# Kernel tuning notes

Measured on AMD Instinct MI355X. Metric: run time of the kernel, lower is better.

## Reference

```python
import jax, jax.numpy as jnp
import numpy as np

B, C, N_ELEM = 16, 256, 8192
N_FILT, N_DIL = 2, 256


def setup_inputs() -> dict:
    key = jax.random.key(0)
    kx, kw = jax.random.split(key)
    x = jax.random.normal(kx, (B, C, N_ELEM), dtype=jnp.float32)
    # xavier_uniform on a (n_out, n_in, n_filt) tensor: fan_in = fan_out = C * N_FILT
    fan = C * N_FILT
    bound = float(np.sqrt(6.0 / (fan + fan)))
    weight = jax.random.uniform(kw, (C, C, N_FILT), minval=-bound, maxval=bound, dtype=jnp.float32)
    return {"x": x, "weight": weight, "n_dil": N_DIL}


def reference(x, weight, n_dil):
    # x: (B, C_in, N); weight: (C_out, C_in, n_filt); requires C_out == C_in.
    n_out, n_in, n_filt = weight.shape
    filter_size = (n_filt - 1) * n_dil + 1
    n_steps = x.shape[2] - filter_size

    # The torch loop computes, for i in [0, n_steps):
    #   x[:, :, i+1] = sum_{c,k} weight[o, c, k] * x_read[:, c, i + k*n_dil]
    # where the k=0 tap reads the UPDATED x (written at step i-1) and all
    # k>=1 taps read the ORIGINAL x (those positions are written at later
    # steps, and torch evaluates the conv before the in-place write).
    # => affine recurrence: s[i+1] = W0 @ s[i] + c[i], s[0] = x[:, :, 0].

    # c[t] = sum_{k>=1} W_k @ x_orig[:, :, t + k*n_dil]  -> (n_steps, B, C_out)
    c = jnp.zeros((n_steps, x.shape[0], n_out), dtype=x.dtype)
    for k in range(1, n_filt):
        xk = x[:, :, k * n_dil: k * n_dil + n_steps]  # (B, C_in, n_steps)
        c = c + jnp.einsum('oc,bct->tbo', weight[:, :, k], xk)

    W0T = weight[:, :, 0].T  # (C_in, C_out)

    def step(state, ct):
        # state: (B, C); ct: (B, C)
        new = state @ W0T + ct
        return new, new

    _, ys = jax.lax.scan(step, x[:, :, 0], c)  # ys: (n_steps, B, C)
    x_out = x.at[:, :, 1:1 + n_steps].set(jnp.transpose(ys, (1, 2, 0)))
    return x_out
```

## Files before the change

### kernel.cpp

```cpp
#include <hip/hip_runtime.h>
#include <stdint.h>


constexpr int BATCH  = 16;
constexpr int CH     = 256;
constexpr int NEL    = 8192;
constexpr int NDIL   = 256;
constexpr int TSTEPS = NEL - (NDIL + 1);
constexpr int LCH    = 16;
constexpr int NCH    = (TSTEPS + LCH - 1) / LCH;
constexpr int OUT_L  = 32;
constexpr int WARM   = 20;
constexpr int NCH2   = (TSTEPS + OUT_L - 1) / OUT_L;
constexpr int TPB    = 256;
constexpr int YPAD   = 260;
constexpr int A2PAD  = 264;
constexpr int TTILES = (TSTEPS + 127) / 128;
constexpr int YROW   = 264;

constexpr size_t OFF_AF    = 0;
constexpr size_t OFF_P1    = OFF_AF    + 256 * 1024;
constexpr size_t OFF_P2    = OFF_P1    + 256 * 1024;
constexpr size_t OFF_AB16  = OFF_P2    + 256 * 1024;
constexpr size_t OFF_W1B   = OFF_AB16  + 128 * 1024;
constexpr size_t OFF_E     = OFF_W1B   + 128 * 1024;
constexpr size_t OFF_INIT  = OFF_E     + (size_t)NCH * BATCH * CH * 4;
constexpr size_t OFF_AFRAG = OFF_INIT  + (size_t)(NCH + 1) * BATCH * CH * 4;
constexpr size_t OFF_W1FR  = OFF_AFRAG + 128 * 1024;
constexpr size_t OFF_CBUF  = OFF_W1FR  + 128 * 1024;
constexpr size_t CBUF_BYTES = (size_t)(NCH * LCH) * BATCH * CH * 2;
constexpr size_t OFF_YBUF  = OFF_CBUF + CBUF_BYTES;
constexpr size_t WS_NEED   = OFF_YBUF + CBUF_BYTES;

typedef __attribute__((ext_vector_type(8))) short bf16x8;
typedef __attribute__((ext_vector_type(4))) float f32x4;

__device__ __forceinline__ float bfu(uint32_t hibits) { return __uint_as_float(hibits); }
__device__ __forceinline__ float bf2f(uint16_t b) { return __uint_as_float(((uint32_t)b) << 16); }
__device__ __forceinline__ uint16_t f2bf(float f) {
  uint32_t u = __float_as_uint(f);
  uint32_t r = u + 0x7fffu + ((u >> 16) & 1u);
  return (uint16_t)(r >> 16);
}

__global__ void k_prep(const float* __restrict__ w, float* __restrict__ Af,
                       uint16_t* __restrict__ Ab, uint16_t* __restrict__ W1b,
                       uint16_t* __restrict__ Afrag, uint16_t* __restrict__ W1f) {
  int o = blockIdx.x, c = threadIdx.x;
  const float2 wv = *(const float2*)&w[(size_t)(o * CH + c) * 2];
  Af[c * CH + o]  = wv.x;
  Ab[c * CH + o]  = f2bf(wv.x);
  W1b[c * CH + o] = f2bf(wv.y);
  if (Afrag) {
    int kb = c >> 5, g = (c >> 3) & 3, ii = c & 7;
    int nt = o >> 4, mm = o & 15;
    size_t idx = (((size_t)(kb * 16 + nt) * 64) + (g * 16 + mm)) * 8 + ii;
    Afrag[idx] = f2bf(wv.x);
    W1f[idx]   = f2bf(wv.y);
  }
}

__global__ void k_init0(const float* __restrict__ x, float* __restrict__ initbuf) {
  int b = blockIdx.x, c = threadIdx.x;
  initbuf[b * CH + c] = x[(size_t)(b * CH + c) * NEL];
}

__global__ __launch_bounds__(TPB) void k_sqmm(const float* __restrict__ in,
                                              float* __restrict__ outm) {
  __shared__ __align__(16) float row[CH];
  int r = blockIdx.x, o = threadIdx.x;
  row[o] = in[r * CH + o];
  __syncthreads();
  float acc = 0.f;
#pragma unroll 8
  for (int k = 0; k < CH; ++k) acc += row[k] * in[k * CH + o];
  outm[r * CH + o] = acc;
}

__global__ void k_edges(const float* __restrict__ x, float* __restrict__ out) {
  size_t base = (size_t)blockIdx.x * NEL;
  int t = threadIdx.x;
  out[base + (NEL - 256) + t] = x[base + (NEL - 256) + t];
  if (t == 0) out[base] = x[base];
}

__global__ __launch_bounds__(512, 4) void k_cgemm_m(const float* __restrict__ x,
                                                    const uint16_t* __restrict__ W1f,
                                                    uint16_t* __restrict__ cb,
                                                    float* __restrict__ out) {
  __shared__ __align__(16) uint16_t Axs[64 * 64 * 8];
  int tid = threadIdx.x, bid = blockIdx.x;
  if (bid >= BATCH * TTILES) {
    int b = bid - BATCH * TTILES;
    int o = tid >> 1, half = tid & 1;
    size_t rbase = (size_t)(b * CH + o) * NEL;
    const float* src = &x[rbase + (NEL - 256) + half * 128];
    float* dst = &out[rbase + (NEL - 256) + half * 128];
#pragma unroll
    for (int i = 0; i < 32; ++i)
      *(float4*)&dst[i * 4] = *(const float4*)&src[i * 4];
    if (half == 0) out[rbase] = x[rbase];
    return;
  }
  int b = bid / TTILES, tt = bid % TTILES;
  int t0 = tt * 128;
  int w = tid >> 6, l = tid & 63, lm = l & 15, g = l >> 4;
  const float* xb = x + (size_t)b * CH * NEL + (t0 + NDIL);

  bf16x8 bv[8][2];
#pragma unroll
  for (int kb = 0; kb < 8; ++kb)
#pragma unroll
    for (int p = 0; p < 2; ++p)
      bv[kb][p] =
          *(const bf16x8*)&W1f[(((size_t)(kb * 16 + w * 2 + p) * 64) + l) * 8];

  int tA = w * 16 + lm;
#pragma unroll
  for (int kq = 0; kq < 4; ++kq) {
    float v[2][8];
#pragma unroll
    for (int k2 = 0; k2 < 2; ++k2)
#pragma unroll
      for (int i = 0; i < 8; ++i)
        v[k2][i] = xb[(size_t)((kq * 2 + k2) * 32 + g * 8 + i) * NEL + tA];
#pragma unroll
    for (int k2 = 0; k2 < 2; ++k2) {
      uint4 pk;
      pk.x = (uint32_t)f2bf(v[k2][0]) | ((uint32_t)f2bf(v[k2][1]) << 16);
      pk.y = (uint32_t)f2bf(v[k2][2]) | ((uint32_t)f2bf(v[k2][3]) << 16);
      pk.z = (uint32_t)f2bf(v[k2][4]) | ((uint32_t)f2bf(v[k2][5]) << 16);
      pk.w = (uint32_t)f2bf(v[k2][6]) | ((uint32_t)f2bf(v[k2][7]) << 16);
      *(uint4*)&Axs[((w * 8 + kq * 2 + k2) * 64 + l) * 8] = pk;
    }
  }
  __syncthreads();

#pragma unroll 1
  for (int mt = 0; mt < 8; ++mt) {
    f32x4 acc0 = (f32x4)0.f, acc1 = (f32x4)0.f;
#pragma unroll
    for (int kb = 0; kb < 8; ++kb) {
      bf16x8 av = *(const bf16x8*)&Axs[((mt * 8 + kb) * 64 + l) * 8];
      acc0 = __builtin_amdgcn_mfma_f32_16x16x32_bf16(av, bv[kb][0], acc0, 0, 0, 0);
      acc1 = __builtin_amdgcn_mfma_f32_16x16x32_bf16(av, bv[kb][1], acc1, 0, 0, 0);
    }
#pragma unroll
    for (int r = 0; r < 4; ++r) {
      int t2 = t0 + mt * 16 + g * 4 + r;
      if (t2 < TSTEPS) {
        size_t base = (size_t)t2 * (BATCH * CH) + b * CH;
        cb[base + (w * 2 + 0) * 16 + lm] = f2bf(acc0[r]);
        cb[base + (w * 2 + 1) * 16 + lm] = f2bf(acc1[r]);
      }
    }
  }
}

__device__ __forceinline__ void scan2_step(
    int t, bool pref, bool doout, const uint16_t* Yr, uint16_t* Yw,
    const uint16_t* __restrict__ cb, uint16_t* __restrict__ yb,
    const bf16x8 af[8][4], ushort* cc, int w, int lm, int g, int tid) {
  bf16x8 yv[8];
#pragma unroll
  for (int kb = 0; kb < 8; ++kb)
    yv[kb] = *(const bf16x8*)&Yr[lm * YROW + kb * 32 + g * 8];
  f32x4 acc[4];
#pragma unroll
  for (int ntl = 0; ntl < 4; ++ntl)
#pragma unroll
    for (int r = 0; r < 4; ++r)
      acc[ntl][r] = bfu(((uint32_t)cc[ntl * 4 + r]) << 16);
  if (pref) {
    size_t cbase = (size_t)(t + 2) * (BATCH * CH);
#pragma unroll
    for (int ntl = 0; ntl < 4; ++ntl)
#pragma unroll
      for (int r = 0; r < 4; ++r)
        cc[ntl * 4 + r] = cb[cbase + (g * 4 + r) * CH + (w * 4 + ntl) * 16 + lm];
  }
#pragma unroll
  for (int ntl = 0; ntl < 4; ++ntl) {
#pragma unroll
    for (int kb = 0; kb < 8; ++kb)
      acc[ntl] = __builtin_amdgcn_mfma_f32_16x16x32_bf16(yv[kb], af[kb][ntl], acc[ntl], 0, 0, 0);
  }
  uint16_t hbv[16];
#pragma unroll
  for (int ntl = 0; ntl < 4; ++ntl)
#pragma unroll
    for (int r = 0; r < 4; ++r) {
      float v = acc[ntl][r];
      int bb = g * 4 + r, o = (w * 4 + ntl) * 16 + lm;
      uint16_t hb = f2bf(v);
      hbv[ntl * 4 + r] = hb;
      Yw[bb * YROW + o] = hb;
    }
  if (doout) {
    uint4 p0, p1;
    p0.x = (uint32_t)hbv[0] | ((uint32_t)hbv[1] << 16);
    p0.y = (uint32_t)hbv[2] | ((uint32_t)hbv[3] << 16);
    p0.z = (uint32_t)hbv[4] | ((uint32_t)hbv[5] << 16);
    p0.w = (uint32_t)hbv[6] | ((uint32_t)hbv[7] << 16);
    p1.x = (uint32_t)hbv[8] | ((uint32_t)hbv[9] << 16);
    p1.y = (uint32_t)hbv[10] | ((uint32_t)hbv[11] << 16);
    p1.z = (uint32_t)hbv[12] | ((uint32_t)hbv[13] << 16);
    p1.w = (uint32_t)hbv[14] | ((uint32_t)hbv[15] << 16);
    uint4* dst = (uint4*)&yb[(size_t)t * 4096 + tid * 16];
    dst[0] = p0;
    dst[1] = p1;
  }
  asm volatile("s_waitcnt lgkmcnt(0)" ::: "memory");
  __builtin_amdgcn_sched_barrier(0);
  __builtin_amdgcn_s_barrier();
  __builtin_amdgcn_sched_barrier(0);
}

__global__ __launch_bounds__(TPB, 2) void k_scan2(
    const uint16_t* __restrict__ Afrag, const uint16_t* __restrict__ cb,
    uint16_t* __restrict__ yb, const float* __restrict__ x) {
  __shared__ __align__(16) uint16_t Y[2][16 * YROW];
  int tid = threadIdx.x;
  int j = blockIdx.x;
  int w = tid >> 6, l = tid & 63;
  int lm = l & 15, g = l >> 4;

  bf16x8 af[8][4];
#pragma unroll
  for (int kb = 0; kb < 8; ++kb)
#pragma unroll
    for (int ntl = 0; ntl < 4; ++ntl) {
      int nt = w * 4 + ntl;
      af[kb][ntl] = *(const bf16x8*)&Afrag[(((size_t)(kb * 16 + nt) * 64) + l) * 8];
    }

  int tstart   = (j == 0) ? 0 : OUT_L * j - WARM;
  int outstart = OUT_L * j;
  int tend     = min(OUT_L * (j + 1), TSTEPS);

  if (j == 0) {
    int b = tid >> 4, o0 = (tid & 15) * 16;
#pragma unroll
    for (int q = 0; q < 16; ++q)
      Y[0][b * YROW + o0 + q] = f2bf(x[(size_t)(b * CH + o0 + q) * NEL]);
  } else {
    for (int q = tid; q < 16 * YROW; q += TPB) Y[0][q] = 0;
  }

  ushort c0[16], c1[16];
  {
#pragma unroll
    for (int ntl = 0; ntl < 4; ++ntl)
#pragma unroll
      for (int r = 0; r < 4; ++r) {
        size_t off = (size_t)(g * 4 + r) * CH + (w * 4 + ntl) * 16 + lm;
        c0[ntl * 4 + r] = cb[(size_t)tstart * (BATCH * CH) + off];
        c1[ntl * 4 + r] = cb[(size_t)(tstart + 1) * (BATCH * CH) + off];
      }
  }
  __syncthreads();

#pragma unroll 1
  for (int ii = 0; ii < OUT_L + WARM + 2; ii += 2) {
    int t = tstart + ii;
    if (t >= tend) break;
    scan2_step(t, t + 2 < tend, t >= outstart, Y[0], Y[1], cb, yb,
               af, c0, w, lm, g, tid);
    if (t + 1 >= tend) break;
    scan2_step(t + 1, t + 3 < tend, t + 1 >= outstart, Y[1], Y[0], cb, yb,
               af, c1, w, lm, g, tid);
  }
}

__global__ __launch_bounds__(TPB) void k_yout(const uint16_t* __restrict__ yb,
                                              float* __restrict__ out) {
  __shared__ __align__(16) uint16_t t2[256 * 72];
  int bid = blockIdx.x;
  int tb = bid >> 4, sub = bid & 15;
  int G = sub >> 2, wS = sub & 3;
  int t0 = tb * 64;
  int tid = threadIdx.x;
  {
    int tl = tid >> 2, part = tid & 3;
    int ty = t0 + tl - 1;
    if (ty >= 0) {
      const uint16_t* src =
          &yb[(size_t)ty * 4096 + (wS * 64 + G * 16) * 16 + part * 64];
#pragma unroll
      for (int i = 0; i < 8; ++i) {
        uint4 vv = *(const uint4*)&src[i * 8];
        uint32_t uu[4] = {vv.x, vv.y, vv.z, vv.w};
        int colb = part * 64 + i * 8;
#pragma unroll
        for (int e = 0; e < 4; ++e) {
          t2[(colb + 2 * e) * 72 + tl]     = (uint16_t)(uu[e] & 0xffffu);
          t2[(colb + 2 * e + 1) * 72 + tl] = (uint16_t)(uu[e] >> 16);
        }
      }
    }
  }
  __syncthreads();
  {
    int b = G * 4 + (tid >> 6);
    int o = wS * 64 + (tid & 63);
    int col = (o & 15) * 16 + ((o >> 4) & 3) * 4 + (b & 3);
    float* dst = &out[(size_t)(b * CH + o) * NEL + t0];
#pragma unroll
    for (int k4 = 0; k4 < 4; ++k4) {
      uint4 v0 = *(const uint4*)&t2[col * 72 + k4 * 16];
      uint4 v1 = *(const uint4*)&t2[col * 72 + k4 * 16 + 8];
      uint32_t uu[8] = {v0.x, v0.y, v0.z, v0.w, v1.x, v1.y, v1.z, v1.w};
      float f[16];
#pragma unroll
      for (int e = 0; e < 8; ++e) {
        f[2 * e]     = bfu(uu[e] << 16);
        f[2 * e + 1] = bfu(uu[e] & 0xffff0000u);
      }
      if (tb == 0 && k4 == 0) {
#pragma unroll
        for (int e = 1; e < 16; ++e) dst[e] = f[e];
      } else {
#pragma unroll
        for (int m = 0; m < 4; ++m)
          *(float4*)&dst[k4 * 16 + m * 4] =
              make_float4(f[4 * m], f[4 * m + 1], f[4 * m + 2], f[4 * m + 3]);
      }
    }
  }
}

__global__ __launch_bounds__(TPB) void k_cgemm_v(const float* __restrict__ x,
                                                 const uint16_t* __restrict__ W1b,
                                                 float* __restrict__ out) {
  __shared__ __align__(16) uint16_t w1[CH * 128];
  __shared__ __align__(16) float xs[32][128];
  int tid = threadIdx.x;
  int bid = blockIdx.x;
  int b = bid / (TTILES * 2);
  int rem = bid % (TTILES * 2);
  int ttile = rem >> 1, otile = rem & 1;
  int t0 = ttile * 128, o0 = otile * 128;
  int tx = tid & 15, ty = tid >> 4;
  int o8 = o0 + tx * 8;
  int tb = t0 + ty * 8;
  {
    uint4* dst = (uint4*)w1;
    for (int q = tid; q < CH * 128 / 8; q += TPB) {
      int row = q >> 4, seg = q & 15;
      dst[q] = *(const uint4*)&W1b[row * CH + o0 + seg * 8];
    }
  }
  float acc[8][8];
#pragma unroll
  for (int i = 0; i < 8; ++i)
#pragma unroll
    for (int j = 0; j < 8; ++j) acc[i][j] = 0.f;
  for (int c0 = 0; c0 < CH; c0 += 32) {
    __syncthreads();
#pragma unroll
    for (int kk = 0; kk < 4; ++kk) {
      int q = tid + kk * TPB;
      int cc = q >> 5, tf = (q & 31) * 4;
      *(float4*)&xs[cc][tf] =
          *(const float4*)&x[(size_t)(b * CH + c0 + cc) * NEL + t0 + NDIL + tf];
    }
    __syncthreads();
#pragma unroll 4
    for (int cc = 0; cc < 32; ++cc) {
      float4 xa = *(const float4*)&xs[cc][ty * 8];
      float4 xb = *(const float4*)&xs[cc][ty * 8 + 4];
      float xv[8] = {xa.x, xa.y, xa.z, xa.w, xb.x, xb.y, xb.z, xb.w};
      uint4 wv = *(const uint4*)&w1[(c0 + cc) * 128 + tx * 8];
      float wf[8] = {bfu(wv.x << 16), bfu(wv.x & 0xffff0000u),
                     bfu(wv.y << 16), bfu(wv.y & 0xffff0000u),
                     bfu(wv.z << 16), bfu(wv.z & 0xffff0000u),
                     bfu(wv.w << 16), bfu(wv.w & 0xffff0000u)};
#pragma unroll
      for (int i = 0; i < 8; ++i)
#pragma unroll
        for (int j = 0; j < 8; ++j) acc[i][j] += xv[i] * wf[j];
    }
  }
#pragma unroll
  for (int j = 0; j < 8; ++j) {
    size_t base = (size_t)(b * CH + o8 + j) * NEL + tb + 1;
#pragma unroll
    for (int i = 0; i < 8; ++i)
      if (tb + i < TSTEPS) out[base + i] = acc[i][j];
  }
}

template <bool PH3>
__global__ __launch_bounds__(TPB) void k_scan(const uint16_t* __restrict__ Ab,
                                              const float* __restrict__ initbuf,
                                              float* __restrict__ Ebuf,
                                              float* __restrict__ out) {
  __shared__ __align__(16) uint16_t Al[CH * CH];
  __shared__ __align__(16) float yl[BATCH * YPAD];
  int tid = threadIdx.x;
  int j = blockIdx.x;
  {
    const uint4* src = (const uint4*)Ab;
    uint4* dst = (uint4*)Al;
    for (int q = tid; q < CH * CH / 8; q += TPB) dst[q] = src[q];
  }
  if constexpr (PH3) {
    for (int q = tid; q < BATCH * CH / 4; q += TPB) {
      int b = q >> 6, c4 = (q & 63) * 4;
      *(float4*)&yl[b * YPAD + c4] =
          *(const float4*)&initbuf[(size_t)j * BATCH * CH + b * CH + c4];
    }
  } else {
    for (int q = tid; q < BATCH * YPAD; q += TPB) yl[q] = 0.f;
  }
  __syncthreads();
  int o4 = (tid & 63) * 4;
  int b4 = (tid >> 6) * 4;
  int len = min(LCH, TSTEPS - j * LCH);
  float acc[4][4];
  for (int i = 0; i < len; ++i) {
    int t = j * LCH + i;
    float cv[4][4];
#pragma unroll
    for (int bb = 0; bb < 4; ++bb)
#pragma unroll
      for (int oo = 0; oo < 4; ++oo)
        cv[bb][oo] = out[(size_t)((b4 + bb) * CH + o4 + oo) * NEL + t + 1];
#pragma unroll
    for (int bb = 0; bb < 4; ++bb)
#pragma unroll
      for (int oo = 0; oo < 4; ++oo) acc[bb][oo] = 0.f;
#pragma unroll 2
    for (int c = 0; c < CH; c += 4) {
      float4 v0 = *(const float4*)&yl[(b4 + 0) * YPAD + c];
      float4 v1 = *(const float4*)&yl[(b4 + 1) * YPAD + c];
      float4 v2 = *(const float4*)&yl[(b4 + 2) * YPAD + c];
      float4 v3 = *(const float4*)&yl[(b4 + 3) * YPAD + c];
      float y0[4] = {v0.x, v0.y, v0.z, v0.w};
      float y1[4] = {v1.x, v1.y, v1.z, v1.w};
      float y2[4] = {v2.x, v2.y, v2.z, v2.w};
      float y3[4] = {v3.x, v3.y, v3.z, v3.w};
#pragma unroll
      for (int k = 0; k < 4; ++k) {
        uint2 au = *(const uint2*)&Al[(c + k) * CH + o4];
        float a[4] = {bfu(au.x << 16), bfu(au.x & 0xffff0000u),
                      bfu(au.y << 16), bfu(au.y & 0xffff0000u)};
#pragma unroll
        for (int oo = 0; oo < 4; ++oo) {
          acc[0][oo] += y0[k] * a[oo];
          acc[1][oo] += y1[k] * a[oo];
          acc[2][oo] += y2[k] * a[oo];
          acc[3][oo] += y3[k] * a[oo];
        }
      }
    }
#pragma unroll
    for (int bb = 0; bb < 4; ++bb)
#pragma unroll
      for (int oo = 0; oo < 4; ++oo) acc[bb][oo] += cv[bb][oo];
    __syncthreads();
#pragma unroll
    for (int bb = 0; bb < 4; ++bb)
      *(float4*)&yl[(b4 + bb) * YPAD + o4] =
          make_float4(acc[bb][0], acc[bb][1], acc[bb][2], acc[bb][3]);
    if constexpr (PH3) {
#pragma unroll
      for (int bb = 0; bb < 4; ++bb)
#pragma unroll
        for (int oo = 0; oo < 4; ++oo)
          out[(size_t)((b4 + bb) * CH + o4 + oo) * NEL + t + 1] = acc[bb][oo];
    }
    __syncthreads();
  }
  if constexpr (!PH3) {
#pragma unroll
    for (int bb = 0; bb < 4; ++bb)
#pragma unroll
      for (int oo = 0; oo < 4; ++oo)
        Ebuf[(size_t)j * BATCH * CH + (b4 + bb) * CH + o4 + oo] = acc[bb][oo];
  }
}

__global__ __launch_bounds__(TPB) void k_phase2(const float* __restrict__ ALf,
                                                const float* __restrict__ Ebuf,
                                                float* __restrict__ initbuf) {
  __shared__ __align__(16) uint16_t At[CH * A2PAD];
  __shared__ __align__(16) float st[CH];
  int b = blockIdx.x, tid = threadIdx.x;
  for (int q = tid; q < CH * CH; q += TPB) {
    int c = q >> 8, o = q & 255;
    At[o * A2PAD + c] = f2bf(ALf[q]);
  }
  st[tid] = initbuf[b * CH + tid];
  __syncthreads();
  for (int jj = 1; jj < NCH; ++jj) {
    float acc = Ebuf[(size_t)(jj - 1) * BATCH * CH + b * CH + tid];
#pragma unroll 4
    for (int c = 0; c < CH; c += 8) {
      uint4 au = *(const uint4*)&At[tid * A2PAD + c];
      float4 s0 = *(const float4*)&st[c];
      float4 s1 = *(const float4*)&st[c + 4];
      acc += bfu(au.x << 16) * s0.x + bfu(au.x & 0xffff0000u) * s0.y +
             bfu(au.y << 16) * s0.z + bfu(au.y & 0xffff0000u) * s0.w +
             bfu(au.z << 16) * s1.x + bfu(au.z & 0xffff0000u) * s1.y +
             bfu(au.w << 16) * s1.z + bfu(au.w & 0xffff0000u) * s1.w;
    }
    __syncthreads();
    st[tid] = acc;
    initbuf[(size_t)jj * BATCH * CH + b * CH + tid] = acc;
    __syncthreads();
  }
}

extern "C" void kernel_launch(void* const* d_in, const int* in_sizes, int n_in,
                              void* d_out, int out_size, void* d_ws, size_t ws_size,
                              hipStream_t stream) {
  const float* x = (const float*)d_in[0];
  const float* w = (const float*)d_in[1];
  float* out = (float*)d_out;
  char* ws = (char*)d_ws;

  float*    Af    = (float*)(ws + OFF_AF);
  float*    P1    = (float*)(ws + OFF_P1);
  float*    P2    = (float*)(ws + OFF_P2);
  uint16_t* Ab    = (uint16_t*)(ws + OFF_AB16);
  uint16_t* W1b   = (uint16_t*)(ws + OFF_W1B);
  float*    Ebuf  = (float*)(ws + OFF_E);
  float*    inb   = (float*)(ws + OFF_INIT);
  uint16_t* Afrag = (uint16_t*)(ws + OFF_AFRAG);
  uint16_t* W1f   = (uint16_t*)(ws + OFF_W1FR);
  uint16_t* cbuf  = (uint16_t*)(ws + OFF_CBUF);
  uint16_t* ybuf  = (uint16_t*)(ws + OFF_YBUF);

  const bool fast = ws_size >= WS_NEED;

  k_prep<<<CH, CH, 0, stream>>>(w, Af, Ab, W1b, fast ? Afrag : nullptr, W1f);
  if (fast) {
    k_cgemm_m<<<BATCH * TTILES + BATCH, 512, 0, stream>>>(x, W1f, cbuf, out);
    k_scan2<<<NCH2, TPB, 0, stream>>>(Afrag, cbuf, ybuf, x);
    k_yout<<<124 * 16, TPB, 0, stream>>>(ybuf, out);
  } else {
    k_edges<<<BATCH * CH, 256, 0, stream>>>(x, out);
    k_init0<<<BATCH, CH, 0, stream>>>(x, inb);
    k_sqmm<<<CH, TPB, 0, stream>>>(Af, P1);
    k_sqmm<<<CH, TPB, 0, stream>>>(P1, P2);
    k_sqmm<<<CH, TPB, 0, stream>>>(P2, P1);
    k_sqmm<<<CH, TPB, 0, stream>>>(P1, P2);
    k_cgemm_v<<<BATCH * TTILES * 2, TPB, 0, stream>>>(x, W1b, out);
    k_scan<false><<<NCH - 1, TPB, 0, stream>>>(Ab, nullptr, Ebuf, out);
    k_phase2<<<BATCH, TPB, 0, stream>>>(P2, Ebuf, inb);
    k_scan<true><<<NCH, TPB, 0, stream>>>(Ab, inb, nullptr, out);
  }
}
```

Measured before the change: 191.9 us.

## Fuse output transpose into scan kernel via LDS ring buffer; halve cgemm time tile

The scan kernel now stages each step's bf16 results in a 16-slot shared-memory ring and, every 16 steps, transposes and writes them straight to the fp32 output. This removes the separate k_yout kernel and the global y buffer round trip. The C-GEMM kernel also moves to 64-step time tiles, launching twice as many blocks with smaller shared memory. The trade-off is 128KB of extra LDS in the scan kernel, which drops it to one block per CU, plus extra barriers during flushes.

Result: slower. 205.1 us (+6.9%).

```diff
diff --git a/kernel.cpp b/kernel.cpp
--- a/kernel.cpp
+++ b/kernel.cpp
@@ -16,6 +16,7 @@
 constexpr int YPAD   = 260;
 constexpr int A2PAD  = 264;
 constexpr int TTILES = (TSTEPS + 127) / 128;
+constexpr int TT64   = 124;
 constexpr int YROW   = 264;
 
 constexpr size_t OFF_AF    = 0;
@@ -29,8 +30,7 @@
 constexpr size_t OFF_W1FR  = OFF_AFRAG + 128 * 1024;
 constexpr size_t OFF_CBUF  = OFF_W1FR  + 128 * 1024;
 constexpr size_t CBUF_BYTES = (size_t)(NCH * LCH) * BATCH * CH * 2;
-constexpr size_t OFF_YBUF  = OFF_CBUF + CBUF_BYTES;
-constexpr size_t WS_NEED   = OFF_YBUF + CBUF_BYTES;
+constexpr size_t WS_NEED   = OFF_CBUF + CBUF_BYTES;
 
 typedef __attribute__((ext_vector_type(8))) short bf16x8;
 typedef __attribute__((ext_vector_type(4))) float f32x4;
@@ -88,10 +88,10 @@
                                                     const uint16_t* __restrict__ W1f,
                                                     uint16_t* __restrict__ cb,
                                                     float* __restrict__ out) {
-  __shared__ __align__(16) uint16_t Axs[64 * 64 * 8];
+  __shared__ __align__(16) uint16_t Axs[32 * 64 * 8];
   int tid = threadIdx.x, bid = blockIdx.x;
-  if (bid >= BATCH * TTILES) {
-    int b = bid - BATCH * TTILES;
+  if (bid >= BATCH * TT64) {
+    int b = bid - BATCH * TT64;
     int o = tid >> 1, half = tid & 1;
     size_t rbase = (size_t)(b * CH + o) * NEL;
     const float* src = &x[rbase + (NEL - 256) + half * 128];
@@ -102,8 +102,8 @@
     if (half == 0) out[rbase] = x[rbase];
     return;
   }
-  int b = bid / TTILES, tt = bid % TTILES;
-  int t0 = tt * 128;
+  int b = bid / TT64, tt = bid % TT64;
+  int t0 = tt * 64;
   int w = tid >> 6, l = tid & 63, lm = l & 15, g = l >> 4;
   const float* xb = x + (size_t)b * CH * NEL + (t0 + NDIL);
 
@@ -115,29 +115,29 @@
       bv[kb][p] =
           *(const bf16x8*)&W1f[(((size_t)(kb * 16 + w * 2 + p) * 64) + l) * 8];
 
-  int tA = w * 16 + lm;
-#pragma unroll
-  for (int kq = 0; kq < 4; ++kq) {
-    float v[2][8];
-#pragma unroll
-    for (int k2 = 0; k2 < 2; ++k2)
+  {
+    int mt_s = w & 3, kb0 = (w >> 2) * 4;
+    int tA = mt_s * 16 + lm;
+    float v[4][8];
+#pragma unroll
+    for (int k2 = 0; k2 < 4; ++k2)
 #pragma unroll
       for (int i = 0; i < 8; ++i)
-        v[k2][i] = xb[(size_t)((kq * 2 + k2) * 32 + g * 8 + i) * NEL + tA];
-#pragma unroll
-    for (int k2 = 0; k2 < 2; ++k2) {
+        v[k2][i] = xb[(size_t)((kb0 + k2) * 32 + g * 8 + i) * NEL + tA];
+#pragma unroll
+    for (int k2 = 0; k2 < 4; ++k2) {
       uint4 pk;
       pk.x = (uint32_t)f2bf(v[k2][0]) | ((uint32_t)f2bf(v[k2][1]) << 16);
       pk.y = (uint32_t)f2bf(v[k2][2]) | ((uint32_t)f2bf(v[k2][3]) << 16);
       pk.z = (uint32_t)f2bf(v[k2][4]) | ((uint32_t)f2bf(v[k2][5]) << 16);
       pk.w = (uint32_t)f2bf(v[k2][6]) | ((uint32_t)f2bf(v[k2][7]) << 16);
-      *(uint4*)&Axs[((w * 8 + kq * 2 + k2) * 64 + l) * 8] = pk;
+      *(uint4*)&Axs[((mt_s * 8 + kb0 + k2) * 64 + l) * 8] = pk;
     }
   }
   __syncthreads();
 
 #pragma unroll 1
-  for (int mt = 0; mt < 8; ++mt) {
+  for (int mt = 0; mt < 4; ++mt) {
     f32x4 acc0 = (f32x4)0.f, acc1 = (f32x4)0.f;
 #pragma unroll
     for (int kb = 0; kb < 8; ++kb) {
@@ -157,9 +157,9 @@
   }
 }
 
-__device__ __forceinline__ void scan2_step(
-    int t, bool pref, bool doout, const uint16_t* Yr, uint16_t* Yw,
-    const uint16_t* __restrict__ cb, uint16_t* __restrict__ yb,
+__device__ __forceinline__ void scan3_step(
+    int t, bool pref, const uint16_t* Yr, uint16_t* Yw,
+    const uint16_t* __restrict__ cb, uint16_t (*R)[4096],
     const bf16x8 af[8][4], ushort* cc, int w, int lm, int g, int tid) {
   bf16x8 yv[8];
 #pragma unroll
@@ -196,7 +196,7 @@
       hbv[ntl * 4 + r] = hb;
       Yw[bb * YROW + o] = hb;
     }
-  if (doout) {
+  {
     uint4 p0, p1;
     p0.x = (uint32_t)hbv[0] | ((uint32_t)hbv[1] << 16);
     p0.y = (uint32_t)hbv[2] | ((uint32_t)hbv[3] << 16);
@@ -206,9 +206,9 @@
     p1.y = (uint32_t)hbv[10] | ((uint32_t)hbv[11] << 16);
     p1.z = (uint32_t)hbv[12] | ((uint32_t)hbv[13] << 16);
     p1.w = (uint32_t)hbv[14] | ((uint32_t)hbv[15] << 16);
-    uint4* dst = (uint4*)&yb[(size_t)t * 4096 + tid * 16];
-    dst[0] = p0;
-    dst[1] = p1;
+    uint16_t* slice = R[t & 15];
+    *(uint4*)&slice[tid * 8] = p0;
+    *(uint4*)&slice[2048 + tid * 8] = p1;
   }
   asm volatile("s_waitcnt lgkmcnt(0)" ::: "memory");
   __builtin_amdgcn_sched_barrier(0);
@@ -216,10 +216,51 @@
   __builtin_amdgcn_sched_barrier(0);
 }
 
-__global__ __launch_bounds__(TPB, 2) void k_scan2(
+__device__ __forceinline__ void scan3_flush(int t, const uint16_t (*R)[4096],
+                                            float* __restrict__ out, int tid) {
+  int ob = t - 14;
+  int o = tid;
+#pragma unroll
+  for (int ii = 0; ii < 16; ii += 2) {
+    int ttw = (o >> 6) * 64 + (ii >> 2) * 16 + (o & 15);
+    int f   = ((o >> 4) & 3) * 4 + (ii & 3);
+    int pos = ((f & 8) ? 2048 : 0) + ttw * 8 + (f & 7);
+    float fa[16], fb[16];
+#pragma unroll
+    for (int q = 0; q < 16; ++q) {
+      uint32_t u = *(const uint32_t*)&R[(q + 15) & 15][pos];
+      fa[q] = bfu(u << 16);
+      fb[q] = bfu(u & 0xffff0000u);
+    }
+    float* dA = &out[(size_t)(ii * CH + o) * NEL + ob];
+    float* dB = &out[(size_t)((ii + 1) * CH + o) * NEL + ob];
+    if (ob == 0) {
+      dA[1] = fa[1]; dA[2] = fa[2]; dA[3] = fa[3];
+      dB[1] = fb[1]; dB[2] = fb[2]; dB[3] = fb[3];
+#pragma unroll
+      for (int m = 1; m < 4; ++m) {
+        *(float4*)&dA[m * 4] = make_float4(fa[4*m], fa[4*m+1], fa[4*m+2], fa[4*m+3]);
+        *(float4*)&dB[m * 4] = make_float4(fb[4*m], fb[4*m+1], fb[4*m+2], fb[4*m+3]);
+      }
+    } else {
+#pragma unroll
+      for (int m = 0; m < 4; ++m) {
+        *(float4*)&dA[m * 4] = make_float4(fa[4*m], fa[4*m+1], fa[4*m+2], fa[4*m+3]);
+        *(float4*)&dB[m * 4] = make_float4(fb[4*m], fb[4*m+1], fb[4*m+2], fb[4*m+3]);
+      }
+    }
+  }
+  asm volatile("s_waitcnt lgkmcnt(0)" ::: "memory");
+  __builtin_amdgcn_sched_barrier(0);
+  __builtin_amdgcn_s_barrier();
+  __builtin_amdgcn_sched_barrier(0);
+}
+
+__global__ __launch_bounds__(TPB, 1) void k_scan3(
     const uint16_t* __restrict__ Afrag, const uint16_t* __restrict__ cb,
-    uint16_t* __restrict__ yb, const float* __restrict__ x) {
+    float* __restrict__ out, const float* __restrict__ x) {
   __shared__ __align__(16) uint16_t Y[2][16 * YROW];
+  __shared__ __align__(16) uint16_t R[16][4096];
   int tid = threadIdx.x;
   int j = blockIdx.x;
   int w = tid >> 6, l = tid & 63;
@@ -236,7 +277,7 @@
 
   int tstart   = (j == 0) ? 0 : OUT_L * j - WARM;
   int outstart = OUT_L * j;
-  int tend     = min(OUT_L * (j + 1), TSTEPS);
+  int tend     = min(OUT_L * j + OUT_L - 1, TSTEPS);
 
   if (j == 0) {
     int b = tid >> 4, o0 = (tid & 15) * 16;
@@ -261,71 +302,14 @@
   __syncthreads();
 
 #pragma unroll 1
-  for (int ii = 0; ii < OUT_L + WARM + 2; ii += 2) {
-    int t = tstart + ii;
+  for (int ii2 = 0; ii2 < OUT_L + WARM + 2; ii2 += 2) {
+    int t = tstart + ii2;
     if (t >= tend) break;
-    scan2_step(t, t + 2 < tend, t >= outstart, Y[0], Y[1], cb, yb,
-               af, c0, w, lm, g, tid);
+    scan3_step(t, t + 2 < tend, Y[0], Y[1], cb, R, af, c0, w, lm, g, tid);
+    if (t >= outstart && (t & 15) == 14) scan3_flush(t, R, out, tid);
     if (t + 1 >= tend) break;
-    scan2_step(t + 1, t + 3 < tend, t + 1 >= outstart, Y[1], Y[0], cb, yb,
-               af, c1, w, lm, g, tid);
-  }
-}
-
-__global__ __launch_bounds__(TPB) void k_yout(const uint16_t* __restrict__ yb,
-                                              float* __restrict__ out) {
-  __shared__ __align__(16) uint16_t t2[256 * 72];
-  int bid = blockIdx.x;
-  int tb = bid >> 4, sub = bid & 15;
-  int G = sub >> 2, wS = sub & 3;
-  int t0 = tb * 64;
-  int tid = threadIdx.x;
-  {
-    int tl = tid >> 2, part = tid & 3;
-    int ty = t0 + tl - 1;
-    if (ty >= 0) {
-      const uint16_t* src =
-          &yb[(size_t)ty * 4096 + (wS * 64 + G * 16) * 16 + part * 64];
-#pragma unroll
-      for (int i = 0; i < 8; ++i) {
-        uint4 vv = *(const uint4*)&src[i * 8];
-        uint32_t uu[4] = {vv.x, vv.y, vv.z, vv.w};
-        int colb = part * 64 + i * 8;
-#pragma unroll
-        for (int e = 0; e < 4; ++e) {
-          t2[(colb + 2 * e) * 72 + tl]     = (uint16_t)(uu[e] & 0xffffu);
-          t2[(colb + 2 * e + 1) * 72 + tl] = (uint16_t)(uu[e] >> 16);
-        }
-      }
-    }
-  }
-  __syncthreads();
-  {
-    int b = G * 4 + (tid >> 6);
-    int o = wS * 64 + (tid & 63);
-    int col = (o & 15) * 16 + ((o >> 4) & 3) * 4 + (b & 3);
-    float* dst = &out[(size_t)(b * CH + o) * NEL + t0];
-#pragma unroll
-    for (int k4 = 0; k4 < 4; ++k4) {
-      uint4 v0 = *(const uint4*)&t2[col * 72 + k4 * 16];
-      uint4 v1 = *(const uint4*)&t2[col * 72 + k4 * 16 + 8];
-      uint32_t uu[8] = {v0.x, v0.y, v0.z, v0.w, v1.x, v1.y, v1.z, v1.w};
-      float f[16];
-#pragma unroll
-      for (int e = 0; e < 8; ++e) {
-        f[2 * e]     = bfu(uu[e] << 16);
-        f[2 * e + 1] = bfu(uu[e] & 0xffff0000u);
-      }
-      if (tb == 0 && k4 == 0) {
-#pragma unroll
-        for (int e = 1; e < 16; ++e) dst[e] = f[e];
-      } else {
-#pragma unroll
-        for (int m = 0; m < 4; ++m)
-          *(float4*)&dst[k4 * 16 + m * 4] =
-              make_float4(f[4 * m], f[4 * m + 1], f[4 * m + 2], f[4 * m + 3]);
-      }
-    }
+    scan3_step(t + 1, t + 3 < tend, Y[1], Y[0], cb, R, af, c1, w, lm, g, tid);
+    if (t + 1 >= outstart && ((t + 1) & 15) == 14) scan3_flush(t + 1, R, out, tid);
   }
 }
 
@@ -530,15 +514,13 @@
   uint16_t* Afrag = (uint16_t*)(ws + OFF_AFRAG);
   uint16_t* W1f   = (uint16_t*)(ws + OFF_W1FR);
   uint16_t* cbuf  = (uint16_t*)(ws + OFF_CBUF);
-  uint16_t* ybuf  = (uint16_t*)(ws + OFF_YBUF);
 
   const bool fast = ws_size >= WS_NEED;
 
   k_prep<<<CH, CH, 0, stream>>>(w, Af, Ab, W1b, fast ? Afrag : nullptr, W1f);
   if (fast) {
-    k_cgemm_m<<<BATCH * TTILES + BATCH, 512, 0, stream>>>(x, W1f, cbuf, out);
-    k_scan2<<<NCH2, TPB, 0, stream>>>(Afrag, cbuf, ybuf, x);
-    k_yout<<<124 * 16, TPB, 0, stream>>>(ybuf, out);
+    k_cgemm_m<<<BATCH * TT64 + BATCH, 512, 0, stream>>>(x, W1f, cbuf, out);
+    k_scan3<<<NCH2, TPB, 0, stream>>>(Afrag, cbuf, out, x);
   } else {
     k_edges<<<BATCH * CH, 256, 0, stream>>>(x, out);
     k_init0<<<BATCH, CH, 0, stream>>>(x, inb);
```
